# Performance work log

Hardware: AMD Instinct MI355X
Metric: run time of the kernel (lower is better)

Reference implementation:

```python
import jax, jax.numpy as jnp
import numpy as np

B, H, S, D = 1, 16, 4096, 64

def setup_inputs() -> dict:
    key = jax.random.key(0)
    kq, kk, kv = jax.random.split(key, 3)
    return {
        "query": jax.random.normal(kq, (B, H, S, D), dtype=jnp.float32),
        "key": jax.random.normal(kk, (B, H, S, D), dtype=jnp.float32),
        "value": jax.random.normal(kv, (B, H, S, D), dtype=jnp.float32),
    }

def reference(query, key, value):
    # qk: [B,H,S,S] materialized score matrix (unfused, as in original)
    qk = jnp.einsum("bhqd,bhkd->bhqk", query, key)
    attn = jax.nn.softmax(qk, axis=-1)
    # dropout_p = 0.0 -> identity
    out = jnp.einsum("bhqk,bhkd->bhqd", attn, value)
    return out
```

## Files before the change

### kernel.cpp

```cpp
#include <hip/hip_runtime.h>
#include <math.h>


#define HH 16
#define SS 4096
#define DDm 64
#define WAVES 8
#define QBW 32
#define QB (WAVES * QBW)
#define KB 64
#define NTL (SS / KB)
#define LDP 72

typedef __attribute__((ext_vector_type(2))) _Float16 half2_t;
typedef __attribute__((ext_vector_type(8))) _Float16 half8_t;
typedef __attribute__((ext_vector_type(16))) float f32x16;

union H8 { half2_t h2[4]; half8_t v; };
union FU { float f; unsigned u; };
union HU { half2_t h; unsigned u; };

__device__ inline unsigned asu(float x){ FU c; c.f=x; return c.u; }
__device__ inline float    asf(unsigned x){ FU c; c.u=x; return c.f; }
__device__ inline unsigned h2u(half2_t x){ HU c; c.h=x; return c.u; }
__device__ inline half2_t  u2h(unsigned x){ HU c; c.u=x; return c.h; }
__device__ inline half2_t  pk2(float a, float b){ half2_t h; h[0]=(_Float16)a; h[1]=(_Float16)b; return h; }

#if __has_builtin(__builtin_amdgcn_permlane32_swap)
#define HAVE_PL32 1
typedef __attribute__((ext_vector_type(2))) unsigned uint2_t;
__device__ inline uint2_t pl32(unsigned a, unsigned b){
  return __builtin_amdgcn_permlane32_swap(a, b, false, false);
}
#else
#define HAVE_PL32 0
#endif

__global__ __launch_bounds__(512, 2)
void attn_fwd(const float* __restrict__ Q, const float* __restrict__ K,
              const float* __restrict__ V, float* __restrict__ O) {
  __shared__ __align__(16) _Float16 Klds[2][KB][LDP];
  __shared__ __align__(16) _Float16 Vt  [2][DDm][LDP];

  const int tid  = threadIdx.x;
  const int lane = tid & 63;
  const int lo5  = lane & 31;
  const int hi   = lane >> 5;

  const int lid  = blockIdx.x;
  const int head = 2 * (lid & 7) + ((lid >> 3) & 1);
  const int qt   = lid >> 4;
  const int qbase = qt * QB + (tid >> 6) * QBW;
  const size_t hoff = (size_t)head * SS * DDm;

  H8 qf[4];
  {
    const float* qp = Q + hoff + (size_t)(qbase + lo5) * DDm;
#pragma unroll
    for (int ds = 0; ds < 4; ++ds) {
      float4 a = *(const float4*)(qp + 16 * ds + 8 * hi);
      float4 b = *(const float4*)(qp + 16 * ds + 8 * hi + 4);
      qf[ds].h2[0] = pk2(a.x, a.y); qf[ds].h2[1] = pk2(a.z, a.w);
      qf[ds].h2[2] = pk2(b.x, b.y); qf[ds].h2[3] = pk2(b.z, b.w);
    }
  }

  const int krow = tid >> 3, kc8 = (tid & 7) * 8;
  const int vd = tid & 63, vk8 = (tid >> 6) * 8;

  float4 ka, kb; float va[8];
  auto issue = [&](int t) {
    const float* kp = K + hoff + (size_t)(t * KB + krow) * DDm + kc8;
    ka = *(const float4*)kp;
    kb = *(const float4*)(kp + 4);
    const float* vp = V + hoff + (size_t)(t * KB + vk8) * DDm + vd;
#pragma unroll
    for (int j = 0; j < 8; ++j) va[j] = vp[j * DDm];
  };
  auto wstage = [&](int buf) {
    H8 kw;
    kw.h2[0] = pk2(ka.x, ka.y); kw.h2[1] = pk2(ka.z, ka.w);
    kw.h2[2] = pk2(kb.x, kb.y); kw.h2[3] = pk2(kb.z, kb.w);
    *(half8_t*)&Klds[buf][krow][kc8] = kw.v;
    H8 vw;
#pragma unroll
    for (int j = 0; j < 4; ++j) vw.h2[j] = pk2(va[2 * j], va[2 * j + 1]);
    *(half8_t*)&Vt[buf][vd][vk8] = vw.v;
  };

  f32x16 acc[2];
#pragma unroll
  for (int nt = 0; nt < 2; ++nt)
#pragma unroll
    for (int r = 0; r < 16; ++r) acc[nt][r] = 0.f;
  float m_run = -INFINITY, l_run = 0.f;

  issue(0); wstage(0); __syncthreads();

  for (int t = 0; t < NTL; ++t) {
    const int cur = t & 1;
    if (t + 1 < NTL) issue(t + 1);

#pragma unroll
    for (int s = 0; s < 2; ++s) {
      const int rs = 32 * s;
      f32x16 st;
#pragma unroll
      for (int r = 0; r < 16; ++r) st[r] = 0.f;
#pragma unroll
      for (int ds = 0; ds < 4; ++ds) {
        half8_t af = *(const half8_t*)&Klds[cur][rs + lo5][16 * ds + 8 * hi];
        st = __builtin_amdgcn_mfma_f32_32x32x16_f16(af, qf[ds].v, st, 0, 0, 0);
      }
      float tmax = st[0];
#pragma unroll
      for (int r = 1; r < 16; ++r) tmax = fmaxf(tmax, st[r]);
#if HAVE_PL32
      { uint2_t pr = pl32(asu(tmax), asu(tmax)); tmax = fmaxf(asf(pr[0]), asf(pr[1])); }
#else
      tmax = fmaxf(tmax, __shfl_xor(tmax, 32, 64));
#endif
      if (__any(tmax > m_run + 8.f)) {
        float mnew = fmaxf(m_run, tmax);
        float corr = __expf(m_run - mnew);
        m_run = mnew; l_run *= corr;
#pragma unroll
        for (int r = 0; r < 16; ++r) {
          const int qr = (r & 3) + 8 * (r >> 2) + 4 * hi;
          float cf = asf(__builtin_amdgcn_ds_bpermute(qr << 2, asu(corr)));
          acc[0][r] *= cf; acc[1][r] *= cf;
        }
      }
      float p[16]; float lsum = 0.f;
#pragma unroll
      for (int r = 0; r < 16; ++r) { p[r] = __expf(st[r] - m_run); lsum += p[r]; }
#if HAVE_PL32
      { uint2_t pr = pl32(asu(lsum), asu(lsum)); lsum = asf(pr[0]) + asf(pr[1]); }
#else
      lsum += __shfl_xor(lsum, 32, 64);
#endif
      l_run += lsum;
      H8 pa[2];
#pragma unroll
      for (int step = 0; step < 2; ++step) {
        const int b = 8 * step;
        half2_t x0 = pk2(p[b + 0], p[b + 1]);
        half2_t x1 = pk2(p[b + 2], p[b + 3]);
        half2_t y0 = pk2(p[b + 4], p[b + 5]);
        half2_t y1 = pk2(p[b + 6], p[b + 7]);
#if HAVE_PL32
        uint2_t sA = pl32(h2u(x0), h2u(y0));
        uint2_t sB = pl32(h2u(x1), h2u(y1));
        pa[step].h2[0] = u2h(sA[0]); pa[step].h2[1] = u2h(sB[0]);
        pa[step].h2[2] = u2h(sA[1]); pa[step].h2[3] = u2h(sB[1]);
#else
        half2_t sx0 = u2h(__shfl_xor(h2u(x0), 32, 64));
        half2_t sx1 = u2h(__shfl_xor(h2u(x1), 32, 64));
        half2_t sy0 = u2h(__shfl_xor(h2u(y0), 32, 64));
        half2_t sy1 = u2h(__shfl_xor(h2u(y1), 32, 64));
        pa[step].h2[0] = hi ? sy0 : x0;  pa[step].h2[1] = hi ? sy1 : x1;
        pa[step].h2[2] = hi ? y0 : sx0;  pa[step].h2[3] = hi ? y1 : sx1;
#endif
      }
#pragma unroll
      for (int step = 0; step < 2; ++step)
#pragma unroll
        for (int nt = 0; nt < 2; ++nt) {
          half8_t vb = *(const half8_t*)&Vt[cur][32 * nt + lo5][rs + 16 * step + 8 * hi];
          acc[nt] = __builtin_amdgcn_mfma_f32_32x32x16_f16(pa[step].v, vb, acc[nt], 0, 0, 0);
        }
    }

    __syncthreads();
    if (t + 1 < NTL) wstage((t + 1) & 1);
    __syncthreads();
  }

  const float invl = 1.f / l_run;
#pragma unroll
  for (int r = 0; r < 16; ++r) {
    const int qr = (r & 3) + 8 * (r >> 2) + 4 * hi;
    float il = asf(__builtin_amdgcn_ds_bpermute(qr << 2, asu(invl)));
    float* op = O + hoff + (size_t)(qbase + qr) * DDm + lo5;
    op[0]  = acc[0][r] * il;
    op[32] = acc[1][r] * il;
  }
}

extern "C" void kernel_launch(void* const* d_in, const int* in_sizes, int n_in,
                              void* d_out, int out_size, void* d_ws, size_t ws_size,
                              hipStream_t stream) {
  const float* Q = (const float*)d_in[0];
  const float* K = (const float*)d_in[1];
  const float* V = (const float*)d_in[2];
  float* O = (float*)d_out;
  attn_fwd<<<dim3(256, 1, 1), dim3(512, 1, 1), 0, stream>>>(Q, K, V, O);
}
```

Baseline: 111.2 us.

## Prepack K/V to fp16 tiles and stream them via async LDS loads

Adds a prepack kernel that converts K and V to fp16 once per call. It writes them into a tile-swizzled workspace layout, with V transposed, that matches the MFMA fragment order. The main attention kernel then fills LDS with global_load_lds in a three-buffer pipeline, needs only one barrier per tile, and preloads all K/V fragments for a tile into registers. It also switches the softmax to exp2 with an fma prescale. This removes the redundant per-block fp32 load and convert work, at the cost of an extra launch and a full pass over K/V through workspace memory. The old kernel remains as a fallback when the workspace is too small.

```diff
diff --git a/kernel.cpp b/kernel.cpp
--- a/kernel.cpp
+++ b/kernel.cpp
@@ -13,6 +13,7 @@
 #define LDP 72
 
 typedef __attribute__((ext_vector_type(2))) _Float16 half2_t;
+typedef __attribute__((ext_vector_type(4))) _Float16 half4_t;
 typedef __attribute__((ext_vector_type(8))) _Float16 half8_t;
 typedef __attribute__((ext_vector_type(16))) float f32x16;
 
@@ -32,13 +33,218 @@
 __device__ inline uint2_t pl32(unsigned a, unsigned b){
   return __builtin_amdgcn_permlane32_swap(a, b, false, false);
 }
-#else
-#define HAVE_PL32 0
-#endif
+#endif
+
+#if __has_builtin(__builtin_amdgcn_exp2f)
+#define EXP2F(x) __builtin_amdgcn_exp2f(x)
+#else
+#define EXP2F(x) exp2f(x)
+#endif
+#define L2E 1.44269504088896f
+
+#define WAITVM(n) asm volatile("s_waitcnt vmcnt(" #n ")" ::: "memory")
+
+__device__ __forceinline__ void gload16(const void* g, void* l) {
+  __builtin_amdgcn_global_load_lds(
+      (const __attribute__((address_space(1))) unsigned int*)g,
+      (__attribute__((address_space(3))) unsigned int*)l, 16, 0, 0);
+}
+
+__global__ __launch_bounds__(256)
+void prepack(const float* __restrict__ K, const float* __restrict__ V,
+             _Float16* __restrict__ Kh, _Float16* __restrict__ Vth) {
+  const int g = blockIdx.x;
+  const int tid = threadIdx.x;
+  if (g < 2048) {
+    const int gt = g * 256 + tid;
+    const int dg = gt & 7, r = (gt >> 3) & 63, t = (gt >> 9) & 63, h = gt >> 15;
+    const float* src = K + ((size_t)(h * SS + t * 64 + r)) * DDm + dg * 8;
+    float4 a = *(const float4*)src;
+    float4 b = *(const float4*)(src + 4);
+    H8 w;
+    w.h2[0] = pk2(a.x, a.y); w.h2[1] = pk2(a.z, a.w);
+    w.h2[2] = pk2(b.x, b.y); w.h2[3] = pk2(b.z, b.w);
+    *(half8_t*)(Kh + (size_t)(h * 64 + t) * 4096 + (dg * 64 + r) * 8) = w.v;
+  } else {
+    const int gt = (g - 2048) * 256 + tid;
+    const int dr = gt & 63, kg = (gt >> 6) & 7, t = (gt >> 9) & 63, h = gt >> 15;
+    const float* src = V + ((size_t)(h * SS + t * 64 + kg * 8)) * DDm + dr;
+    H8 w;
+#pragma unroll
+    for (int j = 0; j < 4; ++j)
+      w.h2[j] = pk2(src[(2 * j) * DDm], src[(2 * j + 1) * DDm]);
+    *(half8_t*)(Vth + (size_t)(h * 64 + t) * 4096 + (kg * 64 + dr) * 8) = w.v;
+  }
+}
 
 __global__ __launch_bounds__(512, 2)
-void attn_fwd(const float* __restrict__ Q, const float* __restrict__ K,
-              const float* __restrict__ V, float* __restrict__ O) {
+void attn_main(const float* __restrict__ Q, const _Float16* __restrict__ Kh,
+               const _Float16* __restrict__ Vth, float* __restrict__ O) {
+  __shared__ __align__(16) _Float16 Kbuf[3][4096];
+  __shared__ __align__(16) _Float16 Vbuf[3][4096];
+
+  const int tid  = threadIdx.x;
+  const int lane = tid & 63;
+  const int lo5  = lane & 31;
+  const int hi   = lane >> 5;
+  const int wv   = tid >> 6;
+
+  const int lid  = blockIdx.x;
+  const int head = 2 * (lid & 7) + ((lid >> 3) & 1);
+  const int qt   = lid >> 4;
+  const int qbase = qt * QB + wv * QBW;
+  const size_t hoff = (size_t)head * SS * DDm;
+
+  H8 qf[4];
+  {
+    const float* qp = Q + hoff + (size_t)(qbase + lo5) * DDm;
+#pragma unroll
+    for (int ds = 0; ds < 4; ++ds) {
+      float4 a = *(const float4*)(qp + 16 * ds + 8 * hi);
+      float4 b = *(const float4*)(qp + 16 * ds + 8 * hi + 4);
+      qf[ds].h2[0] = pk2(a.x, a.y); qf[ds].h2[1] = pk2(a.z, a.w);
+      qf[ds].h2[2] = pk2(b.x, b.y); qf[ds].h2[3] = pk2(b.z, b.w);
+    }
+  }
+
+  const _Float16* kt0 = Kh + (size_t)head * 64 * 4096;
+  const _Float16* vt0 = Vth + (size_t)head * 64 * 4096;
+
+  f32x16 acc[2];
+#pragma unroll
+  for (int nt = 0; nt < 2; ++nt)
+#pragma unroll
+    for (int r = 0; r < 16; ++r) acc[nt][r] = 0.f;
+  float m_run = -INFINITY, l_run = 0.f;
+
+  gload16(kt0 + (size_t)tid * 8, &Kbuf[0][wv * 512]);
+  gload16(vt0 + (size_t)tid * 8, &Vbuf[0][wv * 512]);
+  gload16(kt0 + 4096 + (size_t)tid * 8, &Kbuf[1][wv * 512]);
+  gload16(vt0 + 4096 + (size_t)tid * 8, &Vbuf[1][wv * 512]);
+
+  int bc = 0;
+  for (int t = 0; t < NTL; ++t) {
+    if (t < NTL - 1) { WAITVM(2); } else { WAITVM(0); }
+    __builtin_amdgcn_s_barrier();
+    __builtin_amdgcn_sched_barrier(0);
+    if (t + 2 < NTL) {
+      int bi = bc + 2; if (bi >= 3) bi -= 3;
+      gload16(kt0 + (size_t)(t + 2) * 4096 + (size_t)tid * 8, &Kbuf[bi][wv * 512]);
+      gload16(vt0 + (size_t)(t + 2) * 4096 + (size_t)tid * 8, &Vbuf[bi][wv * 512]);
+    }
+
+    half8_t kf[2][4];
+#pragma unroll
+    for (int s = 0; s < 2; ++s)
+#pragma unroll
+      for (int ds = 0; ds < 4; ++ds)
+        kf[s][ds] = *(const half8_t*)&Kbuf[bc][((ds * 2 + hi) * 64 + 32 * s + lo5) * 8];
+    half8_t vfr[2][2][2];
+#pragma unroll
+    for (int s = 0; s < 2; ++s)
+#pragma unroll
+      for (int sp = 0; sp < 2; ++sp)
+#pragma unroll
+        for (int nt = 0; nt < 2; ++nt)
+          vfr[s][sp][nt] = *(const half8_t*)&Vbuf[bc][(((s * 2 + sp) * 2 + hi) * 64 + nt * 32 + lo5) * 8];
+
+#pragma unroll
+    for (int s = 0; s < 2; ++s) {
+      f32x16 st;
+#pragma unroll
+      for (int r = 0; r < 16; ++r) st[r] = 0.f;
+#pragma unroll
+      for (int ds = 0; ds < 4; ++ds)
+        st = __builtin_amdgcn_mfma_f32_32x32x16_f16(kf[s][ds], qf[ds].v, st, 0, 0, 0);
+
+      float a0 = fmaxf(st[0], st[1]),   a1 = fmaxf(st[2], st[3]);
+      float a2 = fmaxf(st[4], st[5]),   a3 = fmaxf(st[6], st[7]);
+      float a4 = fmaxf(st[8], st[9]),   a5 = fmaxf(st[10], st[11]);
+      float a6 = fmaxf(st[12], st[13]), a7 = fmaxf(st[14], st[15]);
+      float b0 = fmaxf(a0, a1), b1 = fmaxf(a2, a3);
+      float b2 = fmaxf(a4, a5), b3 = fmaxf(a6, a7);
+      float tmax = fmaxf(fmaxf(b0, b1), fmaxf(b2, b3));
+#if HAVE_PL32
+      { uint2_t pr = pl32(asu(tmax), asu(tmax)); tmax = fmaxf(asf(pr[0]), asf(pr[1])); }
+#else
+      tmax = fmaxf(tmax, __shfl_xor(tmax, 32, 64));
+#endif
+      if (__any(tmax > m_run + 8.f)) {
+        float mnew = fmaxf(m_run, tmax);
+        float corr = EXP2F((m_run - mnew) * L2E);
+        m_run = mnew; l_run *= corr;
+#pragma unroll
+        for (int r = 0; r < 16; ++r) {
+          const int qr = (r & 3) + 8 * (r >> 2) + 4 * hi;
+          float cf = asf(__builtin_amdgcn_ds_bpermute(qr << 2, asu(corr)));
+          acc[0][r] *= cf; acc[1][r] *= cf;
+        }
+      }
+
+      const float mt = m_run * L2E;
+      float p[16];
+      float s0 = 0.f, s1 = 0.f, s2 = 0.f, s3 = 0.f;
+#pragma unroll
+      for (int r = 0; r < 16; r += 4) {
+        p[r]     = EXP2F(__builtin_fmaf(st[r],     L2E, -mt)); s0 += p[r];
+        p[r + 1] = EXP2F(__builtin_fmaf(st[r + 1], L2E, -mt)); s1 += p[r + 1];
+        p[r + 2] = EXP2F(__builtin_fmaf(st[r + 2], L2E, -mt)); s2 += p[r + 2];
+        p[r + 3] = EXP2F(__builtin_fmaf(st[r + 3], L2E, -mt)); s3 += p[r + 3];
+      }
+      float lsum = (s0 + s1) + (s2 + s3);
+#if HAVE_PL32
+      { uint2_t pr = pl32(asu(lsum), asu(lsum)); lsum = asf(pr[0]) + asf(pr[1]); }
+#else
+      lsum += __shfl_xor(lsum, 32, 64);
+#endif
+      l_run += lsum;
+
+      H8 pa[2];
+#pragma unroll
+      for (int step = 0; step < 2; ++step) {
+        const int b = 8 * step;
+        half2_t x0 = pk2(p[b + 0], p[b + 1]);
+        half2_t x1 = pk2(p[b + 2], p[b + 3]);
+        half2_t y0 = pk2(p[b + 4], p[b + 5]);
+        half2_t y1 = pk2(p[b + 6], p[b + 7]);
+#if HAVE_PL32
+        uint2_t sA = pl32(h2u(x0), h2u(y0));
+        uint2_t sB = pl32(h2u(x1), h2u(y1));
+        pa[step].h2[0] = u2h(sA[0]); pa[step].h2[1] = u2h(sB[0]);
+        pa[step].h2[2] = u2h(sA[1]); pa[step].h2[3] = u2h(sB[1]);
+#else
+        half2_t sx0 = u2h(__shfl_xor(h2u(x0), 32, 64));
+        half2_t sx1 = u2h(__shfl_xor(h2u(x1), 32, 64));
+        half2_t sy0 = u2h(__shfl_xor(h2u(y0), 32, 64));
+        half2_t sy1 = u2h(__shfl_xor(h2u(y1), 32, 64));
+        pa[step].h2[0] = hi ? sy0 : x0;  pa[step].h2[1] = hi ? sy1 : x1;
+        pa[step].h2[2] = hi ? y0 : sx0;  pa[step].h2[3] = hi ? y1 : sx1;
+#endif
+      }
+#pragma unroll
+      for (int step = 0; step < 2; ++step)
+#pragma unroll
+        for (int nt = 0; nt < 2; ++nt)
+          acc[nt] = __builtin_amdgcn_mfma_f32_32x32x16_f16(pa[step].v, vfr[s][step][nt], acc[nt], 0, 0, 0);
+    }
+
+    bc += 1; if (bc >= 3) bc = 0;
+  }
+
+  const float invl = 1.f / l_run;
+#pragma unroll
+  for (int r = 0; r < 16; ++r) {
+    const int qr = (r & 3) + 8 * (r >> 2) + 4 * hi;
+    float il = asf(__builtin_amdgcn_ds_bpermute(qr << 2, asu(invl)));
+    float* op = O + hoff + (size_t)(qbase + qr) * DDm + lo5;
+    op[0]  = acc[0][r] * il;
+    op[32] = acc[1][r] * il;
+  }
+}
+
+__global__ __launch_bounds__(512, 2)
+void attn_fwd_fb(const float* __restrict__ Q, const float* __restrict__ K,
+                 const float* __restrict__ V, float* __restrict__ O) {
   __shared__ __align__(16) _Float16 Klds[2][KB][LDP];
   __shared__ __align__(16) _Float16 Vt  [2][DDm][LDP];
 
@@ -194,5 +400,13 @@
   const float* K = (const float*)d_in[1];
   const float* V = (const float*)d_in[2];
   float* O = (float*)d_out;
-  attn_fwd<<<dim3(256, 1, 1), dim3(512, 1, 1), 0, stream>>>(Q, K, V, O);
-}
+  const size_t need = (size_t)2 * HH * SS * DDm * sizeof(_Float16);
+  if (ws_size >= need) {
+    _Float16* Kh  = (_Float16*)d_ws;
+    _Float16* Vth = Kh + (size_t)HH * SS * DDm;
+    prepack<<<dim3(4096), dim3(256), 0, stream>>>(K, V, Kh, Vth);
+    attn_main<<<dim3(256), dim3(512), 0, stream>>>(Q, Kh, Vth, O);
+  } else {
+    attn_fwd_fb<<<dim3(256), dim3(512), 0, stream>>>(Q, K, V, O);
+  }
+}
```

Result: slower. 115.2 us (+3.7%).

## Split KV across blocks with fp16 prepack, async LDS loads, and merge kernel

Applied to the files above, without the earlier changes.

Adds a prepack kernel that converts K and V to fp16 in an MFMA-fragment-friendly tiled layout (V transposed). The main kernel splits the KV range into up to four segments per query tile to raise block count and occupancy, and loads tiles straight into LDS with global_load_lds double buffering instead of register staging. A merge kernel combines the partial outputs using the per-segment max and sum. The exponentials are also rewritten as exp2 with a folded log2e. This trades two extra launches and workspace traffic for partial results against more parallelism and less per-iteration conversion work.

```diff
diff --git a/kernel.cpp b/kernel.cpp
--- a/kernel.cpp
+++ b/kernel.cpp
@@ -5,12 +5,8 @@
 #define HH 16
 #define SS 4096
 #define DDm 64
-#define WAVES 8
-#define QBW 32
-#define QB (WAVES * QBW)
 #define KB 64
 #define NTL (SS / KB)
-#define LDP 72
 
 typedef __attribute__((ext_vector_type(2))) _Float16 half2_t;
 typedef __attribute__((ext_vector_type(8))) _Float16 half8_t;
@@ -32,26 +28,73 @@
 __device__ inline uint2_t pl32(unsigned a, unsigned b){
   return __builtin_amdgcn_permlane32_swap(a, b, false, false);
 }
-#else
-#define HAVE_PL32 0
-#endif
-
-__global__ __launch_bounds__(512, 2)
-void attn_fwd(const float* __restrict__ Q, const float* __restrict__ K,
-              const float* __restrict__ V, float* __restrict__ O) {
-  __shared__ __align__(16) _Float16 Klds[2][KB][LDP];
-  __shared__ __align__(16) _Float16 Vt  [2][DDm][LDP];
+#endif
+
+#if __has_builtin(__builtin_amdgcn_exp2f)
+#define EXP2F(x) __builtin_amdgcn_exp2f(x)
+#else
+#define EXP2F(x) exp2f(x)
+#endif
+#define L2E 1.44269504088896f
+
+#define WAITVM(n) asm volatile("s_waitcnt vmcnt(" #n ")" ::: "memory")
+
+__device__ __forceinline__ void gload16(const void* g, void* l) {
+  __builtin_amdgcn_global_load_lds(
+      (const __attribute__((address_space(1))) unsigned int*)g,
+      (__attribute__((address_space(3))) unsigned int*)l, 16, 0, 0);
+}
+
+__global__ __launch_bounds__(256)
+void prepack(const float* __restrict__ K, const float* __restrict__ V,
+             _Float16* __restrict__ Kh, _Float16* __restrict__ Vth) {
+  const int g = blockIdx.x;
+  const int tid = threadIdx.x;
+  if (g < 2048) {
+    const int gt = g * 256 + tid;
+    const int dg = gt & 7, r = (gt >> 3) & 63, t = (gt >> 9) & 63, h = gt >> 15;
+    const float* src = K + ((size_t)(h * SS + t * 64 + r)) * DDm + dg * 8;
+    float4 a = *(const float4*)src;
+    float4 b = *(const float4*)(src + 4);
+    H8 w;
+    w.h2[0] = pk2(a.x, a.y); w.h2[1] = pk2(a.z, a.w);
+    w.h2[2] = pk2(b.x, b.y); w.h2[3] = pk2(b.z, b.w);
+    *(half8_t*)(Kh + (size_t)(h * 64 + t) * 4096 + (dg * 64 + r) * 8) = w.v;
+  } else {
+    const int gt = (g - 2048) * 256 + tid;
+    const int dr = gt & 63, kg = (gt >> 6) & 7, t = (gt >> 9) & 63, h = gt >> 15;
+    const float* src = V + ((size_t)(h * SS + t * 64 + kg * 8)) * DDm + dr;
+    H8 w;
+#pragma unroll
+    for (int j = 0; j < 4; ++j)
+      w.h2[j] = pk2(src[(2 * j) * DDm], src[(2 * j + 1) * DDm]);
+    *(half8_t*)(Vth + (size_t)(h * 64 + t) * 4096 + (kg * 64 + dr) * 8) = w.v;
+  }
+}
+
+__global__ __launch_bounds__(512, 4)
+void attn_split(const float* __restrict__ Q, const _Float16* __restrict__ Kh,
+                const _Float16* __restrict__ Vth, float* __restrict__ Pacc,
+                float* __restrict__ Pml, int nsplit) {
+  __shared__ __align__(16) _Float16 Kbuf[2][4096];
+  __shared__ __align__(16) _Float16 Vbuf[2][4096];
 
   const int tid  = threadIdx.x;
   const int lane = tid & 63;
   const int lo5  = lane & 31;
   const int hi   = lane >> 5;
-
-  const int lid  = blockIdx.x;
-  const int head = 2 * (lid & 7) + ((lid >> 3) & 1);
-  const int qt   = lid >> 4;
-  const int qbase = qt * QB + (tid >> 6) * QBW;
+  const int wv   = tid >> 6;
+
+  const int lid    = blockIdx.x;
+  const int seg    = lid >> 8;
+  const int within = lid & 255;
+  const int head   = 2 * (within & 7) + ((within >> 3) & 1);
+  const int qt     = within >> 4;
+  const int qbase  = qt * 256 + wv * 32;
   const size_t hoff = (size_t)head * SS * DDm;
+
+  const int t0 = (seg * NTL) / nsplit;
+  const int t1 = ((seg + 1) * NTL) / nsplit;
 
   H8 qf[4];
   {
@@ -65,28 +108,10 @@
     }
   }
 
-  const int krow = tid >> 3, kc8 = (tid & 7) * 8;
-  const int vd = tid & 63, vk8 = (tid >> 6) * 8;
-
-  float4 ka, kb; float va[8];
-  auto issue = [&](int t) {
-    const float* kp = K + hoff + (size_t)(t * KB + krow) * DDm + kc8;
-    ka = *(const float4*)kp;
-    kb = *(const float4*)(kp + 4);
-    const float* vp = V + hoff + (size_t)(t * KB + vk8) * DDm + vd;
-#pragma unroll
-    for (int j = 0; j < 8; ++j) va[j] = vp[j * DDm];
-  };
-  auto wstage = [&](int buf) {
-    H8 kw;
-    kw.h2[0] = pk2(ka.x, ka.y); kw.h2[1] = pk2(ka.z, ka.w);
-    kw.h2[2] = pk2(kb.x, kb.y); kw.h2[3] = pk2(kb.z, kb.w);
-    *(half8_t*)&Klds[buf][krow][kc8] = kw.v;
-    H8 vw;
-#pragma unroll
-    for (int j = 0; j < 4; ++j) vw.h2[j] = pk2(va[2 * j], va[2 * j + 1]);
-    *(half8_t*)&Vt[buf][vd][vk8] = vw.v;
-  };
+  const _Float16* kt0 = Kh + (size_t)head * 64 * 4096;
+  const _Float16* vt0 = Vth + (size_t)head * 64 * 4096;
+
+  const int fb = (hi * 64 + lo5) * 8;
 
   f32x16 acc[2];
 #pragma unroll
@@ -95,26 +120,35 @@
     for (int r = 0; r < 16; ++r) acc[nt][r] = 0.f;
   float m_run = -INFINITY, l_run = 0.f;
 
-  issue(0); wstage(0); __syncthreads();
-
-  for (int t = 0; t < NTL; ++t) {
-    const int cur = t & 1;
-    if (t + 1 < NTL) issue(t + 1);
+  gload16(kt0 + (size_t)t0 * 4096 + (size_t)tid * 8, &Kbuf[0][wv * 512]);
+  gload16(vt0 + (size_t)t0 * 4096 + (size_t)tid * 8, &Vbuf[0][wv * 512]);
+  gload16(kt0 + (size_t)(t0 + 1) * 4096 + (size_t)tid * 8, &Kbuf[1][wv * 512]);
+  gload16(vt0 + (size_t)(t0 + 1) * 4096 + (size_t)tid * 8, &Vbuf[1][wv * 512]);
+
+  for (int t = t0; t < t1; ++t) {
+    const int cur = (t - t0) & 1;
+    if (t + 1 < t1) { WAITVM(2); } else { WAITVM(0); }
+    __builtin_amdgcn_s_barrier();
+    __builtin_amdgcn_sched_barrier(0);
 
 #pragma unroll
     for (int s = 0; s < 2; ++s) {
-      const int rs = 32 * s;
       f32x16 st;
 #pragma unroll
       for (int r = 0; r < 16; ++r) st[r] = 0.f;
 #pragma unroll
       for (int ds = 0; ds < 4; ++ds) {
-        half8_t af = *(const half8_t*)&Klds[cur][rs + lo5][16 * ds + 8 * hi];
-        st = __builtin_amdgcn_mfma_f32_32x32x16_f16(af, qf[ds].v, st, 0, 0, 0);
-      }
-      float tmax = st[0];
-#pragma unroll
-      for (int r = 1; r < 16; ++r) tmax = fmaxf(tmax, st[r]);
+        half8_t kf = *(const half8_t*)&Kbuf[cur][ds * 1024 + s * 256 + fb];
+        st = __builtin_amdgcn_mfma_f32_32x32x16_f16(kf, qf[ds].v, st, 0, 0, 0);
+      }
+
+      float a0 = fmaxf(st[0], st[1]),   a1 = fmaxf(st[2], st[3]);
+      float a2 = fmaxf(st[4], st[5]),   a3 = fmaxf(st[6], st[7]);
+      float a4 = fmaxf(st[8], st[9]),   a5 = fmaxf(st[10], st[11]);
+      float a6 = fmaxf(st[12], st[13]), a7 = fmaxf(st[14], st[15]);
+      float b0 = fmaxf(a0, a1), b1 = fmaxf(a2, a3);
+      float b2 = fmaxf(a4, a5), b3 = fmaxf(a6, a7);
+      float tmax = fmaxf(fmaxf(b0, b1), fmaxf(b2, b3));
 #if HAVE_PL32
       { uint2_t pr = pl32(asu(tmax), asu(tmax)); tmax = fmaxf(asf(pr[0]), asf(pr[1])); }
 #else
@@ -122,7 +156,7 @@
 #endif
       if (__any(tmax > m_run + 8.f)) {
         float mnew = fmaxf(m_run, tmax);
-        float corr = __expf(m_run - mnew);
+        float corr = EXP2F((m_run - mnew) * L2E);
         m_run = mnew; l_run *= corr;
 #pragma unroll
         for (int r = 0; r < 16; ++r) {
@@ -131,60 +165,99 @@
           acc[0][r] *= cf; acc[1][r] *= cf;
         }
       }
-      float p[16]; float lsum = 0.f;
-#pragma unroll
-      for (int r = 0; r < 16; ++r) { p[r] = __expf(st[r] - m_run); lsum += p[r]; }
+
+      const float mt = m_run * L2E;
+      float s0 = 0.f, s1 = 0.f, s2 = 0.f, s3 = 0.f;
+#pragma unroll
+      for (int r = 0; r < 16; r += 4) {
+        st[r]     = EXP2F(__builtin_fmaf(st[r],     L2E, -mt)); s0 += st[r];
+        st[r + 1] = EXP2F(__builtin_fmaf(st[r + 1], L2E, -mt)); s1 += st[r + 1];
+        st[r + 2] = EXP2F(__builtin_fmaf(st[r + 2], L2E, -mt)); s2 += st[r + 2];
+        st[r + 3] = EXP2F(__builtin_fmaf(st[r + 3], L2E, -mt)); s3 += st[r + 3];
+      }
+      float lsum = (s0 + s1) + (s2 + s3);
 #if HAVE_PL32
       { uint2_t pr = pl32(asu(lsum), asu(lsum)); lsum = asf(pr[0]) + asf(pr[1]); }
 #else
       lsum += __shfl_xor(lsum, 32, 64);
 #endif
       l_run += lsum;
-      H8 pa[2];
+
 #pragma unroll
       for (int step = 0; step < 2; ++step) {
         const int b = 8 * step;
-        half2_t x0 = pk2(p[b + 0], p[b + 1]);
-        half2_t x1 = pk2(p[b + 2], p[b + 3]);
-        half2_t y0 = pk2(p[b + 4], p[b + 5]);
-        half2_t y1 = pk2(p[b + 6], p[b + 7]);
+        half2_t x0 = pk2(st[b + 0], st[b + 1]);
+        half2_t x1 = pk2(st[b + 2], st[b + 3]);
+        half2_t y0 = pk2(st[b + 4], st[b + 5]);
+        half2_t y1 = pk2(st[b + 6], st[b + 7]);
+        H8 pa;
 #if HAVE_PL32
         uint2_t sA = pl32(h2u(x0), h2u(y0));
         uint2_t sB = pl32(h2u(x1), h2u(y1));
-        pa[step].h2[0] = u2h(sA[0]); pa[step].h2[1] = u2h(sB[0]);
-        pa[step].h2[2] = u2h(sA[1]); pa[step].h2[3] = u2h(sB[1]);
+        pa.h2[0] = u2h(sA[0]); pa.h2[1] = u2h(sB[0]);
+        pa.h2[2] = u2h(sA[1]); pa.h2[3] = u2h(sB[1]);
 #else
         half2_t sx0 = u2h(__shfl_xor(h2u(x0), 32, 64));
         half2_t sx1 = u2h(__shfl_xor(h2u(x1), 32, 64));
         half2_t sy0 = u2h(__shfl_xor(h2u(y0), 32, 64));
         half2_t sy1 = u2h(__shfl_xor(h2u(y1), 32, 64));
-        pa[step].h2[0] = hi ? sy0 : x0;  pa[step].h2[1] = hi ? sy1 : x1;
-        pa[step].h2[2] = hi ? y0 : sx0;  pa[step].h2[3] = hi ? y1 : sx1;
-#endif
-      }
-#pragma unroll
-      for (int step = 0; step < 2; ++step)
+        pa.h2[0] = hi ? sy0 : x0;  pa.h2[1] = hi ? sy1 : x1;
+        pa.h2[2] = hi ? y0 : sx0;  pa.h2[3] = hi ? y1 : sx1;
+#endif
 #pragma unroll
         for (int nt = 0; nt < 2; ++nt) {
-          half8_t vb = *(const half8_t*)&Vt[cur][32 * nt + lo5][rs + 16 * step + 8 * hi];
-          acc[nt] = __builtin_amdgcn_mfma_f32_32x32x16_f16(pa[step].v, vb, acc[nt], 0, 0, 0);
+          half8_t vf = *(const half8_t*)&Vbuf[cur][(s * 2 + step) * 1024 + nt * 256 + fb];
+          acc[nt] = __builtin_amdgcn_mfma_f32_32x32x16_f16(pa.v, vf, acc[nt], 0, 0, 0);
         }
+      }
     }
 
-    __syncthreads();
-    if (t + 1 < NTL) wstage((t + 1) & 1);
-    __syncthreads();
-  }
-
-  const float invl = 1.f / l_run;
+    __builtin_amdgcn_s_barrier();
+    if (t + 2 < t1) {
+      gload16(kt0 + (size_t)(t + 2) * 4096 + (size_t)tid * 8, &Kbuf[cur][wv * 512]);
+      gload16(vt0 + (size_t)(t + 2) * 4096 + (size_t)tid * 8, &Vbuf[cur][wv * 512]);
+    }
+  }
+
+  const int pidx = (head * 16 + qt) * nsplit + seg;
+  float* pa = Pacc + (size_t)pidx * 16384;
 #pragma unroll
   for (int r = 0; r < 16; ++r) {
     const int qr = (r & 3) + 8 * (r >> 2) + 4 * hi;
-    float il = asf(__builtin_amdgcn_ds_bpermute(qr << 2, asu(invl)));
-    float* op = O + hoff + (size_t)(qbase + qr) * DDm + lo5;
-    op[0]  = acc[0][r] * il;
-    op[32] = acc[1][r] * il;
-  }
+    float* op = pa + (wv * 32 + qr) * 64 + lo5;
+    op[0]  = acc[0][r];
+    op[32] = acc[1][r];
+  }
+  if (hi == 0) {
+    Pml[(size_t)pidx * 512 + wv * 32 + lo5]       = m_run;
+    Pml[(size_t)pidx * 512 + 256 + wv * 32 + lo5] = l_run;
+  }
+}
+
+__global__ __launch_bounds__(256)
+void merge_ns(const float* __restrict__ Pacc, const float* __restrict__ Pml,
+              float* __restrict__ O, int nsplit) {
+  const int e  = (blockIdx.x * 256 + threadIdx.x) * 4;
+  const int d4 = e & 63;
+  const int q  = (e >> 6) & 255;
+  const int p  = e >> 14;
+  float m = -INFINITY;
+  for (int s = 0; s < nsplit; ++s)
+    m = fmaxf(m, Pml[(size_t)(p * nsplit + s) * 512 + q]);
+  float den = 0.f;
+  float ox = 0.f, oy = 0.f, oz = 0.f, ow = 0.f;
+  for (int s = 0; s < nsplit; ++s) {
+    const float ms = Pml[(size_t)(p * nsplit + s) * 512 + q];
+    const float ls = Pml[(size_t)(p * nsplit + s) * 512 + 256 + q];
+    const float f  = EXP2F((ms - m) * L2E);
+    den += ls * f;
+    float4 x = *(const float4*)(Pacc + (size_t)(p * nsplit + s) * 16384 + q * 64 + d4);
+    ox += x.x * f; oy += x.y * f; oz += x.z * f; ow += x.w * f;
+  }
+  const float inv = 1.f / den;
+  float4 o; o.x = ox * inv; o.y = oy * inv; o.z = oz * inv; o.w = ow * inv;
+  const int head = p >> 4, qt = p & 15;
+  *(float4*)(O + ((size_t)head * SS + qt * 256 + q) * DDm + d4) = o;
 }
 
 extern "C" void kernel_launch(void* const* d_in, const int* in_sizes, int n_in,
@@ -194,5 +267,23 @@
   const float* K = (const float*)d_in[1];
   const float* V = (const float*)d_in[2];
   float* O = (float*)d_out;
-  attn_fwd<<<dim3(256, 1, 1), dim3(512, 1, 1), 0, stream>>>(Q, K, V, O);
-}
+
+  const size_t n_kv    = (size_t)HH * SS * DDm;
+  const size_t sz_pre  = 2 * n_kv * sizeof(_Float16);
+  const size_t acc_per = (size_t)256 * 16384 * 4;
+  const size_t ml_per  = (size_t)256 * 512 * 4;
+
+  int nsplit = 0;
+  for (int s = 4; s >= 1; --s)
+    if (ws_size >= sz_pre + (size_t)s * (acc_per + ml_per)) { nsplit = s; break; }
+  if (nsplit == 0) nsplit = 1;
+
+  _Float16* Kh  = (_Float16*)d_ws;
+  _Float16* Vth = Kh + n_kv;
+  float* Pacc = (float*)((char*)d_ws + sz_pre);
+  float* Pml  = (float*)((char*)d_ws + sz_pre + (size_t)nsplit * acc_per);
+
+  prepack<<<dim3(4096), dim3(256), 0, stream>>>(K, V, Kh, Vth);
+  attn_split<<<dim3(256 * nsplit), dim3(512), 0, stream>>>(Q, Kh, Vth, Pacc, Pml, nsplit);
+  merge_ns<<<dim3(4096), dim3(256), 0, stream>>>(Pacc, Pml, O, nsplit);
+}
```

After: 128.8 us. 1.16x slower.
